# Kernel tuning notes

Hardware: AMD Instinct MI355X
Metric: run time of the kernel (lower is better)

The kernel has to match this reference:

```python
import jax, jax.numpy as jnp
import numpy as np

MARGIN = 0.3


def setup_inputs() -> dict:
    key = jax.random.key(0)
    k1, k2 = jax.random.split(key)
    inputs = jax.random.normal(k1, (8192, 128), dtype=jnp.float32)
    targets = jax.random.randint(k2, (8192,), 0, 512, dtype=jnp.int64)
    return {"inputs": inputs, "targets": targets}


def reference(inputs, targets):
    # inputs: [n, d], targets: [n]
    sq = jnp.sum(inputs * inputs, axis=1)  # [n]
    # dist[i,j] = ||x_i||^2 + ||x_j||^2 - 2 x_i . x_j
    dist = sq[:, None] + sq[None, :] - 2.0 * (inputs @ inputs.T)
    dist = jnp.sqrt(jnp.clip(dist, 1e-12, None))  # [n, n]
    mask = targets[:, None] == targets[None, :]  # True where same label
    # batch-hard mining: hardest positive (max) and hardest negative (min) per row.
    # Diagonal is always True, so every row has at least one positive.
    dist_ap = jnp.max(jnp.where(mask, dist, -jnp.inf), axis=1)  # [n]
    dist_an = jnp.min(jnp.where(mask, jnp.inf, dist), axis=1)  # [n]
    # MarginRankingLoss with y=1: mean(max(0, margin - (dist_an - dist_ap)))
    loss = jnp.mean(jnp.maximum(0.0, MARGIN - (dist_an - dist_ap)))
    prec = jnp.mean((dist_an > dist_ap).astype(jnp.float32))
    return loss, prec
```

## Files before the change

### kernel.cpp

```cpp
#include <hip/hip_runtime.h>
#include <hip/hip_bf16.h>
#include <math.h>

#define N 8192
#define D 128
#define MARGIN 0.3f

#define TI 128
#define TJ 128
#define JCH 8
#define JT_PER (N / (TJ * JCH))

typedef float f32x4 __attribute__((ext_vector_type(4)));
typedef short bf16x8 __attribute__((ext_vector_type(8)));
typedef unsigned short u16x8 __attribute__((ext_vector_type(8)));

#define AS1 __attribute__((address_space(1)))
#define AS3 __attribute__((address_space(3)))

__device__ inline void gload_lds16(const void* g, void* l) {
    __builtin_amdgcn_global_load_lds((AS1 void*)(void*)(g), (AS3 void*)(l), 16, 0, 0);
}

__device__ inline unsigned short f2bf(float f) {
    unsigned u = __float_as_uint(f);
    unsigned r = (u + 0x7FFFu + ((u >> 16) & 1u)) >> 16;
    return (unsigned short)r;
}

__global__ __launch_bounds__(256) void convert_kernel(const float* __restrict__ X,
                                                      unsigned short* __restrict__ Xb,
                                                      float* __restrict__ sq) {
    int tid = threadIdx.x;
    int row = blockIdx.x * 16 + (tid >> 4);
    int l = tid & 15;
    const float4* p = reinterpret_cast<const float4*>(X + (size_t)row * D + l * 8);
    float4 u = p[0];
    float4 v = p[1];
    float s = u.x*u.x + u.y*u.y + u.z*u.z + u.w*u.w
            + v.x*v.x + v.y*v.y + v.z*v.z + v.w*v.w;
    u16x8 o;
    o[0] = f2bf(u.x); o[1] = f2bf(u.y); o[2] = f2bf(u.z); o[3] = f2bf(u.w);
    o[4] = f2bf(v.x); o[5] = f2bf(v.y); o[6] = f2bf(v.z); o[7] = f2bf(v.w);
    *reinterpret_cast<u16x8*>(Xb + (size_t)row * D + l * 8) = o;
    #pragma unroll
    for (int off = 8; off >= 1; off >>= 1) s += __shfl_xor(s, off);
    if (l == 0) sq[row] = s;
}

__global__ __launch_bounds__(256, 2) void triplet_main(
        const unsigned short* __restrict__ Xb,
        const int* __restrict__ lbl,
        const float* __restrict__ sq,
        unsigned* __restrict__ ap2,
        unsigned* __restrict__ an2) {
    __shared__ unsigned short As[TI * D];
    __shared__ unsigned short Bs[TJ * D];
    __shared__ float sqj_s[TJ];
    __shared__ int   lblj_s[TJ];

    const int tid = threadIdx.x;
    const int w = tid >> 6;
    const int lane = tid & 63;
    const int wr = w >> 1;
    const int wc = w & 1;
    const int quad = lane >> 4;
    const int lx = lane & 15;
    const int i0 = blockIdx.x * TI;

    int lbl_i[16];
    #pragma unroll
    for (int t = 0; t < 4; ++t)
        #pragma unroll
        for (int v = 0; v < 4; ++v)
            lbl_i[t * 4 + v] = lbl[i0 + wr * 64 + t * 16 + quad * 4 + v];

    float m_ap[16], m_an[16];
    #pragma unroll
    for (int q = 0; q < 16; ++q) { m_ap[q] = -INFINITY; m_an[q] = INFINITY; }

    #pragma unroll
    for (int t = 0; t < 8; ++t) {
        int rbase = w * 32 + t * 4;
        int r = rbase + quad;
        int gc = lx ^ (r & 7);
        gload_lds16(Xb + (size_t)(i0 + r) * D + gc * 8, &As[rbase * D]);
    }

    #pragma unroll 1
    for (int jt = 0; jt < JT_PER; ++jt) {
        const int jb = (blockIdx.y * JT_PER + jt) * TJ;
        __syncthreads();

        #pragma unroll
        for (int t = 0; t < 8; ++t) {
            int rbase = w * 32 + t * 4;
            int r = rbase + quad;
            int gc = lx ^ (r & 7);
            gload_lds16(Xb + (size_t)(jb + r) * D + gc * 8, &Bs[rbase * D]);
        }
        if (tid < TJ) { sqj_s[tid] = sq[jb + tid]; lblj_s[tid] = lbl[jb + tid]; }
        __syncthreads();

        f32x4 acc[4][4];
        #pragma unroll
        for (int a = 0; a < 4; ++a)
            #pragma unroll
            for (int b = 0; b < 4; ++b)
                acc[a][b] = (f32x4){0.f, 0.f, 0.f, 0.f};

        #pragma unroll
        for (int ks = 0; ks < 4; ++ks) {
            bf16x8 af[4], bf[4];
            #pragma unroll
            for (int t = 0; t < 4; ++t) {
                int rA = wr * 64 + t * 16 + lx;
                int sc = (ks * 4 + quad) ^ (rA & 7);
                af[t] = *reinterpret_cast<const bf16x8*>(&As[rA * D + sc * 8]);
            }
            #pragma unroll
            for (int t = 0; t < 4; ++t) {
                int rB = wc * 64 + t * 16 + lx;
                int sc = (ks * 4 + quad) ^ (rB & 7);
                bf[t] = *reinterpret_cast<const bf16x8*>(&Bs[rB * D + sc * 8]);
            }
            #pragma unroll
            for (int tr = 0; tr < 4; ++tr)
                #pragma unroll
                for (int tc = 0; tc < 4; ++tc)
                    acc[tr][tc] = __builtin_amdgcn_mfma_f32_16x16x32_bf16(
                        af[tr], bf[tc], acc[tr][tc], 0, 0, 0);
        }

        #pragma unroll
        for (int tc = 0; tc < 4; ++tc) {
            int cj = wc * 64 + tc * 16 + lx;
            int ljv = lblj_s[cj];
            float sjv = sqj_s[cj];
            #pragma unroll
            for (int tr = 0; tr < 4; ++tr) {
                #pragma unroll
                for (int v = 0; v < 4; ++v) {
                    float val = fmaf(-2.f, acc[tr][tc][v], sjv);
                    bool same = (ljv == lbl_i[tr * 4 + v]);
                    int q = tr * 4 + v;
                    m_ap[q] = same ? fmaxf(m_ap[q], val) : m_ap[q];
                    m_an[q] = same ? m_an[q] : fminf(m_an[q], val);
                }
            }
        }
    }

    #pragma unroll
    for (int off = 8; off >= 1; off >>= 1) {
        #pragma unroll
        for (int q = 0; q < 16; ++q) {
            m_ap[q] = fmaxf(m_ap[q], __shfl_xor(m_ap[q], off));
            m_an[q] = fminf(m_an[q], __shfl_xor(m_an[q], off));
        }
    }
    if (lx == 0) {
        #pragma unroll
        for (int t = 0; t < 4; ++t) {
            #pragma unroll
            for (int v = 0; v < 4; ++v) {
                int row = i0 + wr * 64 + t * 16 + quad * 4 + v;
                float si = sq[row];
                float vap = fmaxf(si + m_ap[t * 4 + v], 1e-12f);
                float van = fmaxf(si + m_an[t * 4 + v], 1e-12f);
                atomicMax(&ap2[row], __float_as_uint(vap));
                atomicMin(&an2[row], __float_as_uint(van));
            }
        }
    }
}

__global__ __launch_bounds__(256) void finalize_kernel(const unsigned* __restrict__ ap2,
                                                       const unsigned* __restrict__ an2,
                                                       float* __restrict__ out) {
    int tid = threadIdx.x;
    float ls = 0.f, ps = 0.f;
    for (int row = tid; row < N; row += 256) {
        float ap = sqrtf(__uint_as_float(ap2[row]));
        float an = sqrtf(__uint_as_float(an2[row]));
        ls += fmaxf(0.f, MARGIN - (an - ap));
        ps += (an > ap) ? 1.f : 0.f;
    }
    #pragma unroll
    for (int off = 32; off >= 1; off >>= 1) {
        ls += __shfl_xor(ls, off);
        ps += __shfl_xor(ps, off);
    }
    __shared__ float red[2][4];
    int w = tid >> 6;
    if ((tid & 63) == 0) { red[0][w] = ls; red[1][w] = ps; }
    __syncthreads();
    if (tid == 0) {
        float L = red[0][0] + red[0][1] + red[0][2] + red[0][3];
        float P = red[1][0] + red[1][1] + red[1][2] + red[1][3];
        out[0] = L / (float)N;
        out[1] = P / (float)N;
    }
}

extern "C" void kernel_launch(void* const* d_in, const int* in_sizes, int n_in,
                              void* d_out, int out_size, void* d_ws, size_t ws_size,
                              hipStream_t stream) {
    const float* X = (const float*)d_in[0];
    const int* lbl = (const int*)d_in[1];
    float* out = (float*)d_out;

    float* sq = (float*)d_ws;
    unsigned* ap2 = (unsigned*)d_ws + N;
    unsigned* an2 = (unsigned*)d_ws + 2 * N;
    unsigned short* Xb = (unsigned short*)((char*)d_ws + 3 * N * sizeof(unsigned));

    hipMemsetAsync(ap2, 0x00, N * sizeof(unsigned), stream);
    hipMemsetAsync(an2, 0x7F, N * sizeof(unsigned), stream);

    convert_kernel<<<N / 16, 256, 0, stream>>>(X, Xb, sq);
    dim3 grid(N / TI, JCH);
    triplet_main<<<grid, 256, 0, stream>>>(Xb, lbl, sq, ap2, an2);
    finalize_kernel<<<1, 256, 0, stream>>>(ap2, an2, out);
}
```

Measured before the change: 106.9 us.

## Double-buffer B tiles, keep A fragments in registers, fold memsets into convert

```diff
diff --git a/kernel.cpp b/kernel.cpp
--- a/kernel.cpp
+++ b/kernel.cpp
@@ -30,7 +30,9 @@
 
 __global__ __launch_bounds__(256) void convert_kernel(const float* __restrict__ X,
                                                       unsigned short* __restrict__ Xb,
-                                                      float* __restrict__ sq) {
+                                                      float* __restrict__ sq,
+                                                      unsigned* __restrict__ ap2,
+                                                      unsigned* __restrict__ an2) {
     int tid = threadIdx.x;
     int row = blockIdx.x * 16 + (tid >> 4);
     int l = tid & 15;
@@ -45,7 +47,11 @@
     *reinterpret_cast<u16x8*>(Xb + (size_t)row * D + l * 8) = o;
     #pragma unroll
     for (int off = 8; off >= 1; off >>= 1) s += __shfl_xor(s, off);
-    if (l == 0) sq[row] = s;
+    if (l == 0) {
+        sq[row] = s;
+        ap2[row] = 0u;
+        an2[row] = 0x7F7F7F7Fu;
+    }
 }
 
 __global__ __launch_bounds__(256, 2) void triplet_main(
@@ -54,10 +60,10 @@
         const float* __restrict__ sq,
         unsigned* __restrict__ ap2,
         unsigned* __restrict__ an2) {
-    __shared__ unsigned short As[TI * D];
-    __shared__ unsigned short Bs[TJ * D];
-    __shared__ float sqj_s[TJ];
-    __shared__ int   lblj_s[TJ];
+    __shared__ unsigned short BufA[TI * D];
+    __shared__ unsigned short BufB[TJ * D];
+    __shared__ float sqj_s[2][TJ];
+    __shared__ int   lblj_s[2][TJ];
 
     const int tid = threadIdx.x;
     const int w = tid >> 6;
@@ -67,6 +73,7 @@
     const int quad = lane >> 4;
     const int lx = lane & 15;
     const int i0 = blockIdx.x * TI;
+    const int jbase = blockIdx.y * JT_PER * TJ;
 
     int lbl_i[16];
     #pragma unroll
@@ -84,23 +91,49 @@
         int rbase = w * 32 + t * 4;
         int r = rbase + quad;
         int gc = lx ^ (r & 7);
-        gload_lds16(Xb + (size_t)(i0 + r) * D + gc * 8, &As[rbase * D]);
-    }
+        gload_lds16(Xb + (size_t)(i0 + r) * D + gc * 8, &BufA[rbase * D]);
+    }
+    #pragma unroll
+    for (int t = 0; t < 8; ++t) {
+        int rbase = w * 32 + t * 4;
+        int r = rbase + quad;
+        int gc = lx ^ (r & 7);
+        gload_lds16(Xb + (size_t)(jbase + r) * D + gc * 8, &BufB[rbase * D]);
+    }
+    if (tid < TJ) { sqj_s[0][tid] = sq[jbase + tid]; lblj_s[0][tid] = lbl[jbase + tid]; }
+    __syncthreads();
+
+    bf16x8 af[4][4];
+    #pragma unroll
+    for (int ks = 0; ks < 4; ++ks)
+        #pragma unroll
+        for (int t = 0; t < 4; ++t) {
+            int rA = wr * 64 + t * 16 + lx;
+            int sc = (ks * 4 + quad) ^ (lx & 7);
+            af[ks][t] = *reinterpret_cast<const bf16x8*>(&BufA[rA * D + sc * 8]);
+        }
+    __syncthreads();
 
     #pragma unroll 1
     for (int jt = 0; jt < JT_PER; ++jt) {
-        const int jb = (blockIdx.y * JT_PER + jt) * TJ;
-        __syncthreads();
-
-        #pragma unroll
-        for (int t = 0; t < 8; ++t) {
-            int rbase = w * 32 + t * 4;
-            int r = rbase + quad;
-            int gc = lx ^ (r & 7);
-            gload_lds16(Xb + (size_t)(jb + r) * D + gc * 8, &Bs[rbase * D]);
-        }
-        if (tid < TJ) { sqj_s[tid] = sq[jb + tid]; lblj_s[tid] = lbl[jb + tid]; }
-        __syncthreads();
+        const int cb = jt & 1;
+        const unsigned short* cur = cb ? BufA : BufB;
+        unsigned short* nxt = cb ? BufB : BufA;
+
+        if (jt + 1 < JT_PER) {
+            const int jb1 = jbase + (jt + 1) * TJ;
+            #pragma unroll
+            for (int t = 0; t < 8; ++t) {
+                int rbase = w * 32 + t * 4;
+                int r = rbase + quad;
+                int gc = lx ^ (r & 7);
+                gload_lds16(Xb + (size_t)(jb1 + r) * D + gc * 8, &nxt[rbase * D]);
+            }
+            if (tid < TJ) {
+                sqj_s[1 - cb][tid] = sq[jb1 + tid];
+                lblj_s[1 - cb][tid] = lbl[jb1 + tid];
+            }
+        }
 
         f32x4 acc[4][4];
         #pragma unroll
@@ -111,32 +144,26 @@
 
         #pragma unroll
         for (int ks = 0; ks < 4; ++ks) {
-            bf16x8 af[4], bf[4];
-            #pragma unroll
-            for (int t = 0; t < 4; ++t) {
-                int rA = wr * 64 + t * 16 + lx;
-                int sc = (ks * 4 + quad) ^ (rA & 7);
-                af[t] = *reinterpret_cast<const bf16x8*>(&As[rA * D + sc * 8]);
-            }
+            bf16x8 bf[4];
             #pragma unroll
             for (int t = 0; t < 4; ++t) {
                 int rB = wc * 64 + t * 16 + lx;
-                int sc = (ks * 4 + quad) ^ (rB & 7);
-                bf[t] = *reinterpret_cast<const bf16x8*>(&Bs[rB * D + sc * 8]);
+                int sc = (ks * 4 + quad) ^ (lx & 7);
+                bf[t] = *reinterpret_cast<const bf16x8*>(&cur[rB * D + sc * 8]);
             }
             #pragma unroll
             for (int tr = 0; tr < 4; ++tr)
                 #pragma unroll
                 for (int tc = 0; tc < 4; ++tc)
                     acc[tr][tc] = __builtin_amdgcn_mfma_f32_16x16x32_bf16(
-                        af[tr], bf[tc], acc[tr][tc], 0, 0, 0);
+                        af[ks][tr], bf[tc], acc[tr][tc], 0, 0, 0);
         }
 
         #pragma unroll
         for (int tc = 0; tc < 4; ++tc) {
             int cj = wc * 64 + tc * 16 + lx;
-            int ljv = lblj_s[cj];
-            float sjv = sqj_s[cj];
+            int ljv = lblj_s[cb][cj];
+            float sjv = sqj_s[cb][cj];
             #pragma unroll
             for (int tr = 0; tr < 4; ++tr) {
                 #pragma unroll
@@ -149,6 +176,7 @@
                 }
             }
         }
+        __syncthreads();
     }
 
     #pragma unroll
@@ -175,12 +203,12 @@
     }
 }
 
-__global__ __launch_bounds__(256) void finalize_kernel(const unsigned* __restrict__ ap2,
-                                                       const unsigned* __restrict__ an2,
-                                                       float* __restrict__ out) {
+__global__ __launch_bounds__(1024) void finalize_kernel(const unsigned* __restrict__ ap2,
+                                                        const unsigned* __restrict__ an2,
+                                                        float* __restrict__ out) {
     int tid = threadIdx.x;
     float ls = 0.f, ps = 0.f;
-    for (int row = tid; row < N; row += 256) {
+    for (int row = tid; row < N; row += 1024) {
         float ap = sqrtf(__uint_as_float(ap2[row]));
         float an = sqrtf(__uint_as_float(an2[row]));
         ls += fmaxf(0.f, MARGIN - (an - ap));
@@ -191,13 +219,14 @@
         ls += __shfl_xor(ls, off);
         ps += __shfl_xor(ps, off);
     }
-    __shared__ float red[2][4];
+    __shared__ float red[2][16];
     int w = tid >> 6;
     if ((tid & 63) == 0) { red[0][w] = ls; red[1][w] = ps; }
     __syncthreads();
     if (tid == 0) {
-        float L = red[0][0] + red[0][1] + red[0][2] + red[0][3];
-        float P = red[1][0] + red[1][1] + red[1][2] + red[1][3];
+        float L = 0.f, P = 0.f;
+        #pragma unroll
+        for (int i = 0; i < 16; ++i) { L += red[0][i]; P += red[1][i]; }
         out[0] = L / (float)N;
         out[1] = P / (float)N;
     }
@@ -215,11 +244,8 @@
     unsigned* an2 = (unsigned*)d_ws + 2 * N;
     unsigned short* Xb = (unsigned short*)((char*)d_ws + 3 * N * sizeof(unsigned));
 
-    hipMemsetAsync(ap2, 0x00, N * sizeof(unsigned), stream);
-    hipMemsetAsync(an2, 0x7F, N * sizeof(unsigned), stream);
-
-    convert_kernel<<<N / 16, 256, 0, stream>>>(X, Xb, sq);
+    convert_kernel<<<N / 16, 256, 0, stream>>>(X, Xb, sq, ap2, an2);
     dim3 grid(N / TI, JCH);
     triplet_main<<<grid, 256, 0, stream>>>(Xb, lbl, sq, ap2, an2);
-    finalize_kernel<<<1, 256, 0, stream>>>(ap2, an2, out);
-}
+    finalize_kernel<<<1, 1024, 0, stream>>>(ap2, an2, out);
+}
```

Result: faster. 94.51 us (-11.6%).
